# Kernel optimization log

Hardware: AMD Instinct MI355X
Metric: run time of the kernel (lower is better)

Reference implementation:

```python
import jax, jax.numpy as jnp
import numpy as np

B, S, D = 8, 4096, 256
L, H = 4, 8
HD = D // H  # head_dim = 32
EPS = 1e-5


def layer_norm(x, gamma, beta):
    mu = jnp.mean(x, axis=-1, keepdims=True)
    var = jnp.mean(jnp.square(x - mu), axis=-1, keepdims=True)
    return (x - mu) * jax.lax.rsqrt(var + EPS) * gamma + beta


def setup_inputs() -> dict:
    key = jax.random.key(0)
    ks = jax.random.split(key, 9)
    sc = 0.02
    x = jax.random.normal(ks[0], (B, S, D), dtype=jnp.float32)
    # per-head projection weights, torch Linear convention: (out=head_dim, in=D)
    Wq = jax.random.normal(ks[1], (L, H, HD, D), dtype=jnp.float32) * sc
    Wk = jax.random.normal(ks[2], (L, H, HD, D), dtype=jnp.float32) * sc
    Wv = jax.random.normal(ks[3], (L, H, HD, D), dtype=jnp.float32) * sc
    W1 = jax.random.normal(ks[4], (L, D, D), dtype=jnp.float32) * sc
    b1 = jax.random.normal(ks[5], (L, D), dtype=jnp.float32) * sc
    W2 = jax.random.normal(ks[6], (L, D, D), dtype=jnp.float32) * sc
    b2 = jax.random.normal(ks[7], (L, D), dtype=jnp.float32) * sc
    gamma = jnp.ones((D,), dtype=jnp.float32)
    beta = jnp.zeros((D,), dtype=jnp.float32)
    return {"processed_grid_repr": x, "Wq": Wq, "Wk": Wk, "Wv": Wv,
            "W1": W1, "b1": b1, "W2": W2, "b2": b2,
            "gamma": gamma, "beta": beta}


def reference(processed_grid_repr, Wq, Wk, Wv, W1, b1, W2, b2, gamma, beta):
    out = processed_grid_repr  # (B, S, D)
    scale = 1.0 / jnp.sqrt(jnp.float32(S))  # original scales by sqrt(seq_len)
    for l in range(L):
        h = layer_norm(out, gamma, beta)
        # all heads at once: (B, H, S, HD)
        Q = jnp.einsum('bsd,hed->bhse', h, Wq[l])
        K = jnp.einsum('bsd,hed->bhse', h, Wk[l])
        V = jnp.einsum('bsd,hed->bhse', h, Wv[l])
        # original does key.reshape(B, HD, S) (a RESHAPE, not a transpose)
        Kr = K.reshape(B, H, HD, S)
        # original einsum 'bqq,bqd->bqd' only uses the diagonal of QK^r,
        # so compute only the diagonal: diag[b,h,q] = sum_e Q[b,h,q,e]*Kr[b,h,e,q]
        diag = jnp.einsum('bhse,bhes->bhs', Q, Kr) * scale
        attn = diag[..., None] * V  # (B, H, S, HD)
        # concat heads along last dim (head order preserved)
        msa_out = attn.transpose(0, 2, 1, 3).reshape(B, S, D)
        attended = msa_out + out
        m = layer_norm(attended, gamma, beta)
        m = jax.nn.gelu(m @ W1[l].T + b1[l], approximate=False)
        m = jax.nn.gelu(m @ W2[l].T + b2[l], approximate=False)
        out = m + attended
    # final: layer norm of CLS-like token 0
    return layer_norm(out[:, 0, :], gamma, beta)  # (B, D)
```

## Files before the change

kernel.cpp:

```cpp
#include <hip/hip_runtime.h>
#include <hip/hip_bf16.h>
#include <hip/hip_fp16.h>

typedef _Float16 half_t;
typedef _Float16 half8 __attribute__((ext_vector_type(8)));
typedef _Float16 half4 __attribute__((ext_vector_type(4)));
typedef float f32x4 __attribute__((ext_vector_type(4)));

#define BB 8
#define SS 4096
#define DD 256
#define HH 8
#define LL 4
#define MTOT (BB*SS)

__device__ inline float gelu_f(float v) { return 0.5f * v * (1.0f + erff(v * 0.70710678118f)); }
__device__ inline half8 splat8(half_t v) { return (half8){v, v, v, v, v, v, v, v}; }

__device__ __forceinline__ void gload16(const half_t* g, half_t* l) {
    __builtin_amdgcn_global_load_lds(
        (const __attribute__((address_space(1))) void*)g,
        (__attribute__((address_space(3))) void*)l, 16, 0, 0);
}

__global__ __launch_bounds__(256) void prep_weights(
    const float* __restrict__ Wq, const float* __restrict__ Wk, const float* __restrict__ Wv,
    const float* __restrict__ W1, const float* __restrict__ b1,
    const float* __restrict__ W2, const float* __restrict__ b2,
    const float* __restrict__ gamma, const float* __restrict__ beta,
    half_t* __restrict__ Wall, half_t* __restrict__ W1h, half_t* __restrict__ W2h,
    float* __restrict__ bqkv, float* __restrict__ b1f, float* __restrict__ b2f)
{
    int blk = blockIdx.x;
    int l = blk / 5, type = blk % 5;
    int o = threadIdx.x;
    const float* src = (type == 0 ? Wq : type == 1 ? Wk : type == 2 ? Wv : type == 3 ? W1 : W2)
                       + ((size_t)l * 256 + o) * 256;
    half_t* dsth = (type < 3) ? Wall + ((size_t)(l * 3 + type) * 256 + o) * 256
                 : (type == 3) ? W1h + ((size_t)l * 256 + o) * 256
                               : W2h + ((size_t)l * 256 + o) * 256;
    float acc = 0.f;
    for (int d4 = 0; d4 < 64; ++d4) {
        float4 w = *(const float4*)(src + d4 * 4);
        half4 hv;
        if (type == 4) {
            hv = half4{ (half_t)w.x, (half_t)w.y, (half_t)w.z, (half_t)w.w };
        } else {
            float4 g = *(const float4*)(gamma + d4 * 4);
            float4 bt = *(const float4*)(beta + d4 * 4);
            acc += w.x * bt.x + w.y * bt.y + w.z * bt.z + w.w * bt.w;
            hv = half4{ (half_t)(w.x * g.x), (half_t)(w.y * g.y), (half_t)(w.z * g.z), (half_t)(w.w * g.w) };
        }
        *(half4*)(dsth + d4 * 4) = hv;
    }
    if (type < 3) bqkv[(l * 3 + type) * 256 + o] = acc;
    else if (type == 3) b1f[l * 256 + o] = b1[l * 256 + o] + acc;
    else b2f[l * 256 + o] = b2[l * 256 + o];
}

__global__ __launch_bounds__(256) void cvt_x_stats(const float* __restrict__ in,
                                                   half_t* __restrict__ out,
                                                   float2* __restrict__ st0,
                                                   float2* __restrict__ st1) {
    int wave = threadIdx.x >> 6, lane = threadIdx.x & 63;
    int row = blockIdx.x * 4 + wave;
    const float* ip = in + (size_t)row * DD + lane * 4;
    float4 v = *(const float4*)ip;
    half4 h = { (half_t)v.x, (half_t)v.y, (half_t)v.z, (half_t)v.w };
    *(half4*)(out + (size_t)row * DD + lane * 4) = h;
    float s1 = v.x + v.y + v.z + v.w;
    float s2 = v.x * v.x + v.y * v.y + v.z * v.z + v.w * v.w;
    #pragma unroll
    for (int m = 32; m; m >>= 1) {
        s1 += __shfl_xor(s1, m);
        s2 += __shfl_xor(s2, m);
    }
    if (lane == 0) {
        st0[row] = make_float2(s1, s2);
        st1[row] = make_float2(0.f, 0.f);
    }
}

__device__ inline void xcd_remap(int& bx, int& by, int& bz) {
    int lin = blockIdx.x + gridDim.x * (blockIdx.y + gridDim.y * blockIdx.z);
    int nyz = gridDim.y * gridDim.z;
    int xcd = lin & 7;
    int slot = lin >> 3;
    int yz = slot % nyz;
    int xi = slot / nyz;
    bx = xcd + 8 * xi;
    by = yz % gridDim.y;
    bz = yz / gridDim.y;
}

template<int NORM, int EPI, int STATS>
__global__ __launch_bounds__(256) void gemm128(const half_t* __restrict__ A,
                                               const float2* __restrict__ st0,
                                               const float2* __restrict__ st1,
                                               const half_t* __restrict__ Wbase,
                                               const float* __restrict__ biasBase,
                                               const half_t* __restrict__ resid,
                                               half_t* __restrict__ o0,
                                               half_t* __restrict__ o1,
                                               half_t* __restrict__ o2,
                                               float2* __restrict__ outSt0,
                                               float2* __restrict__ outSt1) {
    const int t = threadIdx.x, lane = t & 63, wavei = t >> 6;
    const int wm = wavei >> 1, wn = wavei & 1, r = lane & 15, g = lane >> 4;
    int bx, by, bz;
    xcd_remap(bx, by, bz);
    const int row0 = bx * 128, col0 = by * 128;
    const half_t* W = Wbase + (size_t)bz * 65536;
    const float* bias = biasBase + bz * 256;
    half_t* outp = (bz == 0) ? o0 : ((bz == 1) ? o1 : o2);

    __shared__ __align__(16) half_t lds[2][16384];

    const half_t* Ag = A + (size_t)row0 * DD;
    const half_t* Wg = W + (size_t)col0 * DD;

    half8 sA[4], bA[4];
    if (NORM) {
        #pragma unroll
        for (int mt = 0; mt < 4; ++mt) {
            int row = row0 + wm * 64 + mt * 16 + r;
            float2 p0 = st0[row], p1 = st1[row];
            float s1 = p0.x + p1.x, s2 = p0.y + p1.y;
            float mu = s1 * (1.0f / DD);
            float var = s2 * (1.0f / DD) - mu * mu;
            float rs = rsqrtf(var + 1e-5f);
            sA[mt] = splat8((half_t)rs);
            bA[mt] = splat8((half_t)(-mu * rs));
        }
    }

    int rowS[4], chS[4];
    #pragma unroll
    for (int i = 0; i < 4; ++i) {
        int G = i * 256 + t;
        rowS[i] = G >> 3;
        chS[i] = ((G & 7) ^ (rowS[i] & 7)) * 8;
    }

    #pragma unroll
    for (int i = 0; i < 4; ++i) {
        int G = i * 256 + t;
        gload16(Ag + (size_t)rowS[i] * DD + chS[i], &lds[0][G * 8]);
        gload16(Wg + (size_t)rowS[i] * DD + chS[i], &lds[0][8192 + G * 8]);
    }
    __syncthreads();

    f32x4 acc[4][4];
    #pragma unroll
    for (int i = 0; i < 4; ++i)
        #pragma unroll
        for (int j = 0; j < 4; ++j) acc[i][j] = (f32x4){0.f, 0.f, 0.f, 0.f};

    #pragma unroll
    for (int stp = 0; stp < 4; ++stp) {
        const int cur = stp & 1;
        if (stp < 3) {
            int kk = (stp + 1) * 64;
            #pragma unroll
            for (int i = 0; i < 4; ++i) {
                int G = i * 256 + t;
                gload16(Ag + (size_t)rowS[i] * DD + kk + chS[i], &lds[cur ^ 1][G * 8]);
                gload16(Wg + (size_t)rowS[i] * DD + kk + chS[i], &lds[cur ^ 1][8192 + G * 8]);
            }
        }
        #pragma unroll
        for (int ks = 0; ks < 2; ++ks) {
            half8 af[4], bf[4];
            #pragma unroll
            for (int mt = 0; mt < 4; ++mt) {
                int rw = wm * 64 + mt * 16 + r;
                int cc = (ks * 4 + g) ^ (rw & 7);
                half8 raw = *(const half8*)&lds[cur][rw * 64 + cc * 8];
                af[mt] = NORM ? (half8)(raw * sA[mt] + bA[mt]) : raw;
            }
            #pragma unroll
            for (int nt = 0; nt < 4; ++nt) {
                int rw = wn * 64 + nt * 16 + r;
                int cc = (ks * 4 + g) ^ (rw & 7);
                bf[nt] = *(const half8*)&lds[cur][8192 + rw * 64 + cc * 8];
            }
            #pragma unroll
            for (int mt = 0; mt < 4; ++mt)
                #pragma unroll
                for (int nt = 0; nt < 4; ++nt)
                    acc[mt][nt] = __builtin_amdgcn_mfma_f32_16x16x32_f16(af[mt], bf[nt], acc[mt][nt], 0, 0, 0);
        }
        __syncthreads();
    }

    half_t* ldsT = &lds[0][0];
    #pragma unroll
    for (int mt = 0; mt < 4; ++mt) {
        #pragma unroll
        for (int nt = 0; nt < 4; ++nt) {
            int colL = wn * 64 + nt * 16 + r;
            float bv = bias[col0 + colL];
            #pragma unroll
            for (int j = 0; j < 4; ++j) {
                int rowL = wm * 64 + mt * 16 + g * 4 + j;
                float v = acc[mt][nt][j] + bv;
                if (EPI != 0) v = gelu_f(v);
                ldsT[rowL * 128 + (colL ^ ((rowL & 12) << 2))] = (half_t)v;
            }
        }
    }
    __syncthreads();
    const int l15 = lane & 15, lg = lane >> 4;
    float2* outSt = (by == 0) ? outSt0 : outSt1;
    #pragma unroll
    for (int i = 0; i < 8; ++i) {
        int rowL = wavei * 32 + lg * 8 + i;
        int colL = l15 * 8;
        half8 v = *(const half8*)&ldsT[rowL * 128 + (colL ^ ((rowL & 12) << 2))];
        size_t off = (size_t)(row0 + rowL) * DD + col0 + colL;
        if (EPI == 2) {
            half8 rsd = *(const half8*)&resid[off];
            #pragma unroll
            for (int q = 0; q < 8; ++q) v[q] = (half_t)((float)v[q] + (float)rsd[q]);
        }
        *(half8*)&outp[off] = v;
        if (STATS) {
            float s1 = 0.f, s2 = 0.f;
            #pragma unroll
            for (int q = 0; q < 8; ++q) { float f = (float)v[q]; s1 += f; s2 += f * f; }
            #pragma unroll
            for (int m = 1; m <= 8; m <<= 1) {
                s1 += __shfl_xor(s1, m);
                s2 += __shfl_xor(s2, m);
            }
            if (l15 == 0) outSt[row0 + rowL] = make_float2(s1, s2);
        }
    }
}

__global__ __launch_bounds__(256) void diag_tiled(const half_t* __restrict__ Q,
                                                  const half_t* __restrict__ K,
                                                  float* __restrict__ dg) {
    int blk = blockIdx.x;
    int sblk = blk & 15, h = (blk >> 4) & 7, b = blk >> 7;
    int t = threadIdx.x;
    __shared__ __align__(16) half_t kt[256 * 32];
    int r0b = sblk * 8;
    {
        int e = t >> 3, del = t & 7;
        const half_t* kp = K + ((size_t)b * SS + e * 128 + r0b + del) * DD + h * 32;
        int4* dst = (int4*)&kt[t * 32];
        const int4* sp = (const int4*)kp;
        dst[0] = sp[0]; dst[1] = sp[1]; dst[2] = sp[2]; dst[3] = sp[3];
    }
    __syncthreads();
    int s = sblk * 256 + t;
    const half8* q8 = (const half8*)(Q + ((size_t)b * SS + s) * DD + h * 32);
    int cs = t & 31, ds = t >> 5;
    float sum = 0.f;
    #pragma unroll
    for (int v = 0; v < 4; ++v) {
        half8 qq = q8[v];
        #pragma unroll
        for (int j = 0; j < 8; ++j) {
            int e = v * 8 + j;
            sum += (float)qq[j] * (float)kt[(e * 8 + ds) * 32 + cs];
        }
    }
    dg[((size_t)b << 15) | ((size_t)h << 12) | s] = sum * 0.015625f;
}

__global__ __launch_bounds__(256) void attn_stat(const half_t* __restrict__ resid,
                                                 const half_t* __restrict__ V,
                                                 const float* __restrict__ dg,
                                                 half_t* __restrict__ att,
                                                 float2* __restrict__ st0,
                                                 float2* __restrict__ st1) {
    int wave = threadIdx.x >> 6, lane = threadIdx.x & 63;
    int row = blockIdx.x * 4 + wave;
    int b = row >> 12, s = row & (SS - 1);
    int h = lane >> 3;
    float dgv = dg[((size_t)b << 15) | ((size_t)h << 12) | s];
    size_t base = (size_t)row * DD + lane * 4;
    half4 rs4 = *(const half4*)(resid + base);
    half4 v4 = *(const half4*)(V + base);
    float a0 = (float)rs4[0] + dgv * (float)v4[0];
    float a1 = (float)rs4[1] + dgv * (float)v4[1];
    float a2 = (float)rs4[2] + dgv * (float)v4[2];
    float a3 = (float)rs4[3] + dgv * (float)v4[3];
    half4 at = { (half_t)a0, (half_t)a1, (half_t)a2, (half_t)a3 };
    *(half4*)(att + base) = at;
    float s1 = a0 + a1 + a2 + a3;
    float s2 = a0 * a0 + a1 * a1 + a2 * a2 + a3 * a3;
    #pragma unroll
    for (int m = 32; m; m >>= 1) {
        s1 += __shfl_xor(s1, m);
        s2 += __shfl_xor(s2, m);
    }
    if (lane == 0) {
        st0[row] = make_float2(s1, s2);
        st1[row] = make_float2(0.f, 0.f);
    }
}

__global__ __launch_bounds__(256) void final_ln_kernel(const half_t* __restrict__ cur,
                                                       float* __restrict__ out,
                                                       const float* __restrict__ gamma,
                                                       const float* __restrict__ beta) {
    int b = blockIdx.x;
    int d = threadIdx.x;
    float x = (float)cur[(size_t)b * SS * DD + d];
    float s1 = x, s2 = x * x;
    #pragma unroll
    for (int m = 32; m; m >>= 1) {
        s1 += __shfl_xor(s1, m);
        s2 += __shfl_xor(s2, m);
    }
    __shared__ float ls1[4], ls2[4];
    int wave = threadIdx.x >> 6, lane = threadIdx.x & 63;
    if (lane == 0) { ls1[wave] = s1; ls2[wave] = s2; }
    __syncthreads();
    float t1 = ls1[0] + ls1[1] + ls1[2] + ls1[3];
    float t2 = ls2[0] + ls2[1] + ls2[2] + ls2[3];
    float mu = t1 * (1.0f / DD);
    float var = t2 * (1.0f / DD) - mu * mu;
    float rs = rsqrtf(var + 1e-5f);
    out[(size_t)b * DD + d] = (x - mu) * rs * gamma[d] + beta[d];
}

extern "C" void kernel_launch(void* const* d_in, const int* in_sizes, int n_in,
                              void* d_out, int out_size, void* d_ws, size_t ws_size,
                              hipStream_t stream) {
    const float* x     = (const float*)d_in[0];
    const float* Wq    = (const float*)d_in[1];
    const float* Wk    = (const float*)d_in[2];
    const float* Wv    = (const float*)d_in[3];
    const float* W1    = (const float*)d_in[4];
    const float* b1    = (const float*)d_in[5];
    const float* W2    = (const float*)d_in[6];
    const float* b2    = (const float*)d_in[7];
    const float* gamma = (const float*)d_in[8];
    const float* beta  = (const float*)d_in[9];

    char* p = (char*)d_ws;
    half_t* x16  = (half_t*)p; p += (size_t)MTOT * DD * 2;
    half_t* cur  = (half_t*)p; p += (size_t)MTOT * DD * 2;
    half_t* att  = (half_t*)p; p += (size_t)MTOT * DD * 2;
    half_t* Qb   = (half_t*)p; p += (size_t)MTOT * DD * 2;
    half_t* Kb   = (half_t*)p; p += (size_t)MTOT * DD * 2;
    half_t* Vb   = (half_t*)p; p += (size_t)MTOT * DD * 2;
    half_t* m1   = (half_t*)p; p += (size_t)MTOT * DD * 2;
    float*  dgp  = (float*)p;  p += (size_t)BB * HH * SS * 4;
    float2* stA0 = (float2*)p; p += (size_t)MTOT * 8;
    float2* stA1 = (float2*)p; p += (size_t)MTOT * 8;
    float2* stB0 = (float2*)p; p += (size_t)MTOT * 8;
    float2* stB1 = (float2*)p; p += (size_t)MTOT * 8;
    half_t* Wall = (half_t*)p; p += (size_t)LL * 3 * 65536 * 2;
    half_t* W1h  = (half_t*)p; p += (size_t)LL * 65536 * 2;
    half_t* W2h  = (half_t*)p; p += (size_t)LL * 65536 * 2;
    float*  bqkv = (float*)p;  p += (size_t)LL * 3 * 256 * 4;
    float*  b1f  = (float*)p;  p += (size_t)LL * 256 * 4;
    float*  b2f  = (float*)p;  p += (size_t)LL * 256 * 4;

    prep_weights<<<LL * 5, 256, 0, stream>>>(Wq, Wk, Wv, W1, b1, W2, b2, gamma, beta,
                                             Wall, W1h, W2h, bqkv, b1f, b2f);
    cvt_x_stats<<<MTOT / 4, 256, 0, stream>>>(x, x16, stA0, stA1);

    const half_t* curin = x16;
    for (int l = 0; l < LL; ++l) {
        gemm128<1, 0, 0><<<dim3(256, 2, 3), 256, 0, stream>>>(
            curin, stA0, stA1, Wall + (size_t)l * 3 * 65536, bqkv + l * 3 * 256,
            nullptr, Qb, Kb, Vb, nullptr, nullptr);
        diag_tiled<<<1024, 256, 0, stream>>>(Qb, Kb, dgp);
        attn_stat<<<MTOT / 4, 256, 0, stream>>>(curin, Vb, dgp, att, stB0, stB1);
        gemm128<1, 1, 0><<<dim3(256, 2, 1), 256, 0, stream>>>(
            att, stB0, stB1, W1h + (size_t)l * 65536, b1f + l * 256,
            nullptr, m1, m1, m1, nullptr, nullptr);
        gemm128<0, 2, 1><<<dim3(256, 2, 1), 256, 0, stream>>>(
            m1, nullptr, nullptr, W2h + (size_t)l * 65536, b2f + l * 256,
            att, cur, cur, cur, stA0, stA1);
        curin = cur;
    }
    final_ln_kernel<<<BB, 256, 0, stream>>>(cur, (float*)d_out, gamma, beta);
}
```

Baseline: 362.1 us.

## Shrink GEMM row tile to 64 and use explicit vmcnt waits with raw barriers

The GEMM kernel now covers 64 rows by 128 columns per block instead of 128x128, which doubles the grid to 512 row blocks and cuts LDS use and accumulator registers. The aim is more resident blocks per CU and better wave coverage across the GPU for these skinny K=256 GEMMs. The prologue barrier is gone, and __syncthreads in the main loop is replaced with explicit s_waitcnt vmcnt counts plus s_barrier and sched_barrier, so prefetches can stay in flight while the current stage is computed. In exchange, each block loads the weight tile for less work, so weight traffic and per-block overhead go up.

```diff
diff --git a/kernel.cpp b/kernel.cpp
--- a/kernel.cpp
+++ b/kernel.cpp
@@ -94,7 +94,7 @@
 }
 
 template<int NORM, int EPI, int STATS>
-__global__ __launch_bounds__(256) void gemm128(const half_t* __restrict__ A,
+__global__ __launch_bounds__(256) void gemm64n(const half_t* __restrict__ A,
                                                const float2* __restrict__ st0,
                                                const float2* __restrict__ st1,
                                                const half_t* __restrict__ Wbase,
@@ -109,21 +109,21 @@
     const int wm = wavei >> 1, wn = wavei & 1, r = lane & 15, g = lane >> 4;
     int bx, by, bz;
     xcd_remap(bx, by, bz);
-    const int row0 = bx * 128, col0 = by * 128;
+    const int row0 = bx * 64, col0 = by * 128;
     const half_t* W = Wbase + (size_t)bz * 65536;
     const float* bias = biasBase + bz * 256;
     half_t* outp = (bz == 0) ? o0 : ((bz == 1) ? o1 : o2);
 
-    __shared__ __align__(16) half_t lds[2][16384];
+    __shared__ __align__(16) half_t lds[2][12288];
 
     const half_t* Ag = A + (size_t)row0 * DD;
     const half_t* Wg = W + (size_t)col0 * DD;
 
-    half8 sA[4], bA[4];
+    half8 sA[2], bA[2];
     if (NORM) {
         #pragma unroll
-        for (int mt = 0; mt < 4; ++mt) {
-            int row = row0 + wm * 64 + mt * 16 + r;
+        for (int mt = 0; mt < 2; ++mt) {
+            int row = row0 + wm * 32 + mt * 16 + r;
             float2 p0 = st0[row], p1 = st1[row];
             float s1 = p0.x + p1.x, s2 = p0.y + p1.y;
             float mu = s1 * (1.0f / DD);
@@ -134,27 +134,32 @@
         }
     }
 
-    int rowS[4], chS[4];
+    int rwA[2], chA[2], rwW[4], chW[4];
+    #pragma unroll
+    for (int i = 0; i < 2; ++i) {
+        int G = i * 256 + t;
+        rwA[i] = G >> 3;
+        chA[i] = ((G & 7) ^ (rwA[i] & 7)) * 8;
+    }
     #pragma unroll
     for (int i = 0; i < 4; ++i) {
         int G = i * 256 + t;
-        rowS[i] = G >> 3;
-        chS[i] = ((G & 7) ^ (rowS[i] & 7)) * 8;
-    }
-
-    #pragma unroll
-    for (int i = 0; i < 4; ++i) {
-        int G = i * 256 + t;
-        gload16(Ag + (size_t)rowS[i] * DD + chS[i], &lds[0][G * 8]);
-        gload16(Wg + (size_t)rowS[i] * DD + chS[i], &lds[0][8192 + G * 8]);
-    }
-    __syncthreads();
-
-    f32x4 acc[4][4];
+        rwW[i] = G >> 3;
+        chW[i] = ((G & 7) ^ (rwW[i] & 7)) * 8;
+    }
+
+    f32x4 acc[2][4];
+    #pragma unroll
+    for (int i = 0; i < 2; ++i)
+        #pragma unroll
+        for (int j = 0; j < 4; ++j) acc[i][j] = (f32x4){0.f, 0.f, 0.f, 0.f};
+
+    #pragma unroll
+    for (int i = 0; i < 2; ++i)
+        gload16(Ag + (size_t)rwA[i] * DD + chA[i], &lds[0][(i * 256 + t) * 8]);
     #pragma unroll
     for (int i = 0; i < 4; ++i)
-        #pragma unroll
-        for (int j = 0; j < 4; ++j) acc[i][j] = (f32x4){0.f, 0.f, 0.f, 0.f};
+        gload16(Wg + (size_t)rwW[i] * DD + chW[i], &lds[0][4096 + (i * 256 + t) * 8]);
 
     #pragma unroll
     for (int stp = 0; stp < 4; ++stp) {
@@ -162,18 +167,23 @@
         if (stp < 3) {
             int kk = (stp + 1) * 64;
             #pragma unroll
-            for (int i = 0; i < 4; ++i) {
-                int G = i * 256 + t;
-                gload16(Ag + (size_t)rowS[i] * DD + kk + chS[i], &lds[cur ^ 1][G * 8]);
-                gload16(Wg + (size_t)rowS[i] * DD + kk + chS[i], &lds[cur ^ 1][8192 + G * 8]);
-            }
-        }
+            for (int i = 0; i < 2; ++i)
+                gload16(Ag + (size_t)rwA[i] * DD + kk + chA[i], &lds[cur ^ 1][(i * 256 + t) * 8]);
+            #pragma unroll
+            for (int i = 0; i < 4; ++i)
+                gload16(Wg + (size_t)rwW[i] * DD + kk + chW[i], &lds[cur ^ 1][4096 + (i * 256 + t) * 8]);
+            asm volatile("s_waitcnt vmcnt(6)" ::: "memory");
+        } else {
+            asm volatile("s_waitcnt vmcnt(0)" ::: "memory");
+        }
+        __builtin_amdgcn_s_barrier();
+        __builtin_amdgcn_sched_barrier(0);
         #pragma unroll
         for (int ks = 0; ks < 2; ++ks) {
-            half8 af[4], bf[4];
-            #pragma unroll
-            for (int mt = 0; mt < 4; ++mt) {
-                int rw = wm * 64 + mt * 16 + r;
+            half8 af[2], bf[4];
+            #pragma unroll
+            for (int mt = 0; mt < 2; ++mt) {
+                int rw = wm * 32 + mt * 16 + r;
                 int cc = (ks * 4 + g) ^ (rw & 7);
                 half8 raw = *(const half8*)&lds[cur][rw * 64 + cc * 8];
                 af[mt] = NORM ? (half8)(raw * sA[mt] + bA[mt]) : raw;
@@ -182,27 +192,28 @@
             for (int nt = 0; nt < 4; ++nt) {
                 int rw = wn * 64 + nt * 16 + r;
                 int cc = (ks * 4 + g) ^ (rw & 7);
-                bf[nt] = *(const half8*)&lds[cur][8192 + rw * 64 + cc * 8];
+                bf[nt] = *(const half8*)&lds[cur][4096 + rw * 64 + cc * 8];
             }
             #pragma unroll
-            for (int mt = 0; mt < 4; ++mt)
+            for (int mt = 0; mt < 2; ++mt)
                 #pragma unroll
                 for (int nt = 0; nt < 4; ++nt)
                     acc[mt][nt] = __builtin_amdgcn_mfma_f32_16x16x32_f16(af[mt], bf[nt], acc[mt][nt], 0, 0, 0);
         }
-        __syncthreads();
+        __builtin_amdgcn_sched_barrier(0);
+        __builtin_amdgcn_s_barrier();
     }
 
     half_t* ldsT = &lds[0][0];
     #pragma unroll
-    for (int mt = 0; mt < 4; ++mt) {
+    for (int mt = 0; mt < 2; ++mt) {
         #pragma unroll
         for (int nt = 0; nt < 4; ++nt) {
             int colL = wn * 64 + nt * 16 + r;
             float bv = bias[col0 + colL];
             #pragma unroll
             for (int j = 0; j < 4; ++j) {
-                int rowL = wm * 64 + mt * 16 + g * 4 + j;
+                int rowL = wm * 32 + mt * 16 + g * 4 + j;
                 float v = acc[mt][nt][j] + bv;
                 if (EPI != 0) v = gelu_f(v);
                 ldsT[rowL * 128 + (colL ^ ((rowL & 12) << 2))] = (half_t)v;
@@ -210,12 +221,12 @@
         }
     }
     __syncthreads();
-    const int l15 = lane & 15, lg = lane >> 4;
     float2* outSt = (by == 0) ? outSt0 : outSt1;
     #pragma unroll
-    for (int i = 0; i < 8; ++i) {
-        int rowL = wavei * 32 + lg * 8 + i;
-        int colL = l15 * 8;
+    for (int i = 0; i < 4; ++i) {
+        int G = i * 256 + t;
+        int rowL = G >> 4;
+        int colL = (G & 15) * 8;
         half8 v = *(const half8*)&ldsT[rowL * 128 + (colL ^ ((rowL & 12) << 2))];
         size_t off = (size_t)(row0 + rowL) * DD + col0 + colL;
         if (EPI == 2) {
@@ -233,7 +244,7 @@
                 s1 += __shfl_xor(s1, m);
                 s2 += __shfl_xor(s2, m);
             }
-            if (l15 == 0) outSt[row0 + rowL] = make_float2(s1, s2);
+            if ((t & 15) == 0) outSt[row0 + rowL] = make_float2(s1, s2);
         }
     }
 }
@@ -368,15 +379,15 @@
 
     const half_t* curin = x16;
     for (int l = 0; l < LL; ++l) {
-        gemm128<1, 0, 0><<<dim3(256, 2, 3), 256, 0, stream>>>(
+        gemm64n<1, 0, 0><<<dim3(512, 2, 3), 256, 0, stream>>>(
             curin, stA0, stA1, Wall + (size_t)l * 3 * 65536, bqkv + l * 3 * 256,
             nullptr, Qb, Kb, Vb, nullptr, nullptr);
         diag_tiled<<<1024, 256, 0, stream>>>(Qb, Kb, dgp);
         attn_stat<<<MTOT / 4, 256, 0, stream>>>(curin, Vb, dgp, att, stB0, stB1);
-        gemm128<1, 1, 0><<<dim3(256, 2, 1), 256, 0, stream>>>(
+        gemm64n<1, 1, 0><<<dim3(512, 2, 1), 256, 0, stream>>>(
             att, stB0, stB1, W1h + (size_t)l * 65536, b1f + l * 256,
             nullptr, m1, m1, m1, nullptr, nullptr);
-        gemm128<0, 2, 1><<<dim3(256, 2, 1), 256, 0, stream>>>(
+        gemm64n<0, 2, 1><<<dim3(512, 2, 1), 256, 0, stream>>>(
             m1, nullptr, nullptr, W2h + (size_t)l * 65536, b2f + l * 256,
             att, cur, cur, cur, stA0, stA1);
         curin = cur;
```

New measurement: 359.7 us. Within noise of the previous version (-0.7%).
